# Kernel tuning notes

Measured on AMD Instinct MI355X. Metric: run time of the kernel, lower is better.

The kernel has to match this reference:

```python
import jax, jax.numpy as jnp
import numpy as np

B, RATIO, IN_CH, H = 32, 32, 64, 8
E = IN_CH * H                 # embed_dim = in_channels * n_heads = 512
NODES_PER_GRAPH = 512
N = B * NODES_PER_GRAPH       # 16384 source nodes


def setup_inputs() -> dict:
    key = jax.random.key(0)
    ks = jax.random.split(key, 6)
    x = jax.random.normal(ks[0], (N, E), dtype=jnp.float32)
    # edge_index is accepted by forward but unused in 'attn' mode
    edge_index = jax.random.randint(ks[1], (2, 262144), 0, N, dtype=jnp.int32)
    # per-node graph id, sorted, equal-size graphs (batch[-1] + 1 == B)
    batch = jnp.repeat(jnp.arange(B, dtype=jnp.int32), NODES_PER_GRAPH)
    # learned params: cluster query seeds + MultiheadAttention in/out projections
    xcent_base = jax.random.normal(ks[2], (RATIO, E), dtype=jnp.float32)
    in_proj_w = jax.random.normal(ks[3], (3 * E, E), dtype=jnp.float32) / np.sqrt(E).astype(np.float32)
    in_proj_b = jnp.zeros((3 * E,), dtype=jnp.float32)
    out_proj_w = jax.random.normal(ks[4], (E, E), dtype=jnp.float32) / np.sqrt(E).astype(np.float32)
    out_proj_b = jnp.zeros((E,), dtype=jnp.float32)
    return dict(x=x, edge_index=edge_index, batch=batch, xcent_base=xcent_base,
                in_proj_w=in_proj_w, in_proj_b=in_proj_b,
                out_proj_w=out_proj_w, out_proj_b=out_proj_b)


def reference(x, edge_index, batch, xcent_base, in_proj_w, in_proj_b, out_proj_w, out_proj_b):
    # BipartPool.forward, mode='attn':
    #   x_aggrs = xcent_base.repeat(batch_size, 1)  -> queries [L, E], L = B*ratio
    #   MultiheadAttention(q=x_aggrs, k=v=x, attn_mask=mask[batch].T)
    # mask[batch].T is True (disallowed) where query's graph != node's graph.
    L = B * RATIO
    head_dim = E // H
    x_aggrs = jnp.tile(xcent_base, (B, 1))                        # [L, E]

    wq, wk, wv = jnp.split(in_proj_w, 3, axis=0)                  # each [E, E]
    bq, bk, bv = jnp.split(in_proj_b, 3, axis=0)
    q = (x_aggrs @ wq.T + bq).reshape(L, H, head_dim).transpose(1, 0, 2)  # [H, L, hd]
    k = (x @ wk.T + bk).reshape(N, H, head_dim).transpose(1, 0, 2)        # [H, N, hd]
    v = (x @ wv.T + bv).reshape(N, H, head_dim).transpose(1, 0, 2)        # [H, N, hd]

    batchcent = jnp.repeat(jnp.arange(B, dtype=batch.dtype), RATIO)       # [L]
    allowed = batchcent[:, None] == batch[None, :]                        # [L, N]

    scale = np.float32(1.0 / np.sqrt(head_dim))
    scores = jnp.einsum('hld,hnd->hln', q, k) * scale                     # [H, L, N]
    scores = jnp.where(allowed[None], scores, -jnp.inf)
    attn = jax.nn.softmax(scores, axis=-1)
    out = jnp.einsum('hln,hnd->hld', attn, v)                             # [H, L, hd]
    out = out.transpose(1, 0, 2).reshape(L, E)
    xcent = out @ out_proj_w.T + out_proj_b                               # [L, E]
    # original returns (xcent.reshape(B, ratio, E), None, None, batchcent, None, None)
    return xcent.reshape(B, RATIO, E), batchcent
```

## Files before the change

### kernel.cpp

```cpp
#include <hip/hip_runtime.h>
#include <hip/hip_bf16.h>

#define NGRAPH 32
#define NHEAD 8
#define EMB 512
#define NNODES 16384
#define NPG 512
#define LQ 1024
#define PST 520
#define GCH 262144

typedef __attribute__((ext_vector_type(8))) short short8;
typedef __attribute__((ext_vector_type(4))) float f32x4;

static __device__ __forceinline__ unsigned short f2bf(float f) {
  union { float f; unsigned u; } v; v.f = f;
  unsigned r = (v.u + 0x7fffu + ((v.u >> 16) & 1u)) >> 16;
  return (unsigned short)r;
}

static __device__ __forceinline__ short8 cvt8(float4 a, float4 b) {
  short8 r;
  r[0] = f2bf(a.x); r[1] = f2bf(a.y); r[2] = f2bf(a.z); r[3] = f2bf(a.w);
  r[4] = f2bf(b.x); r[5] = f2bf(b.y); r[6] = f2bf(b.z); r[7] = f2bf(b.w);
  return r;
}

static __device__ __forceinline__ void gload_lds16(const ushort* g, ushort* l) {
  __builtin_amdgcn_global_load_lds(
      (const __attribute__((address_space(1))) unsigned*)g,
      (__attribute__((address_space(3))) unsigned*)l, 16, 0, 0);
}

#define BARRIER_LGKM()                                        \
  do {                                                        \
    asm volatile("s_waitcnt lgkmcnt(0)" ::: "memory");        \
    __builtin_amdgcn_s_barrier();                             \
  } while (0)

__global__ __launch_bounds__(256) void prep_all(
    const float* __restrict__ x, const float* __restrict__ wv,
    const float* __restrict__ wo, const float* __restrict__ wq,
    const float* __restrict__ wk, const float* __restrict__ xc,
    const float* __restrict__ bq,
    ushort* __restrict__ xbC, ushort* __restrict__ xbTC,
    ushort* __restrict__ wvb, ushort* __restrict__ wob,
    ushort* __restrict__ PCb, float* __restrict__ bcent) {
  __shared__ ushort smemU[11776];
  const int b = blockIdx.x;
  const int t = threadIdx.x;

  if (b < 32) {
    ushort* Qs  = smemU;
    ushort* WkT = smemU + 2304;
    int h = b >> 2, qs = b & 3;
    int w = t >> 6, lane = t & 63;
    int lr = lane & 15, grp = lane >> 4, ko = grp * 8;

    {
      int dl = t >> 2, cq = t & 3;
      const float* wr = wk + (long)(h * 64 + dl) * EMB + qs * 128;
#pragma unroll
      for (int m = 0; m < 8; ++m) {
        int c0 = cq * 32 + m * 4;
        float4 v = *reinterpret_cast<const float4*>(wr + c0);
        WkT[(c0 + 0) * 72 + dl] = f2bf(0.125f * v.x);
        WkT[(c0 + 1) * 72 + dl] = f2bf(0.125f * v.y);
        WkT[(c0 + 2) * 72 + dl] = f2bf(0.125f * v.z);
        WkT[(c0 + 3) * 72 + dl] = f2bf(0.125f * v.w);
      }
    }

    f32x4 qa[2];
    qa[0] = (f32x4)(0.0f); qa[1] = (f32x4)(0.0f);
#pragma unroll 4
    for (int kk = 0; kk < EMB; kk += 32) {
      const float* xr0 = xc + lr * EMB + kk + ko;
      const float* xr1 = xc + (16 + lr) * EMB + kk + ko;
      const float* wr  = wq + (long)(h * 64 + w * 16 + lr) * EMB + kk + ko;
      short8 a0 = cvt8(*reinterpret_cast<const float4*>(xr0),
                       *reinterpret_cast<const float4*>(xr0 + 4));
      short8 a1 = cvt8(*reinterpret_cast<const float4*>(xr1),
                       *reinterpret_cast<const float4*>(xr1 + 4));
      short8 bb = cvt8(*reinterpret_cast<const float4*>(wr),
                       *reinterpret_cast<const float4*>(wr + 4));
      qa[0] = __builtin_amdgcn_mfma_f32_16x16x32_bf16(a0, bb, qa[0], 0, 0, 0);
      qa[1] = __builtin_amdgcn_mfma_f32_16x16x32_bf16(a1, bb, qa[1], 0, 0, 0);
    }
    float bias = bq[h * 64 + w * 16 + lr];
#pragma unroll
    for (int i = 0; i < 2; ++i)
#pragma unroll
      for (int r = 0; r < 4; ++r)
        Qs[(i * 16 + grp * 4 + r) * 72 + w * 16 + lr] = f2bf(qa[i][r] + bias);
    __syncthreads();

    f32x4 pa[2][2];
#pragma unroll
    for (int i = 0; i < 2; ++i)
#pragma unroll
      for (int j = 0; j < 2; ++j) pa[i][j] = (f32x4)(0.0f);
#pragma unroll
    for (int kk = 0; kk < 64; kk += 32) {
      short8 a0 = *reinterpret_cast<const short8*>(&Qs[lr * 72 + kk + ko]);
      short8 a1 = *reinterpret_cast<const short8*>(&Qs[(16 + lr) * 72 + kk + ko]);
#pragma unroll
      for (int j = 0; j < 2; ++j) {
        short8 bb = *reinterpret_cast<const short8*>(
            &WkT[(w * 32 + j * 16 + lr) * 72 + kk + ko]);
        pa[0][j] = __builtin_amdgcn_mfma_f32_16x16x32_bf16(a0, bb, pa[0][j], 0, 0, 0);
        pa[1][j] = __builtin_amdgcn_mfma_f32_16x16x32_bf16(a1, bb, pa[1][j], 0, 0, 0);
      }
    }
#pragma unroll
    for (int i = 0; i < 2; ++i)
#pragma unroll
      for (int j = 0; j < 2; ++j)
#pragma unroll
        for (int r = 0; r < 4; ++r)
          PCb[(long)(h * 32 + i * 16 + grp * 4 + r) * EMB + qs * 128 + w * 32 + j * 16 + lr] =
              f2bf(pa[i][j][r]);
    return;
  }

  if (b < 1056) {
    ushort* tileA = smemU;
    ushort* tileB = smemU + 4608;
    int local = b - 32;
    int xr = local & 7, j = local >> 3;
    int m = j >> 5, r = j & 31;
    int g = xr + 8 * m;
    int bc = r & 7;
    int bl = r >> 3;
    int n0 = bl * 128, e0 = bc * 64;
    int trr = t >> 4, tc = t & 15;

    float4 vA[4], vB[4];
#pragma unroll
    for (int p = 0; p < 4; ++p)
      vA[p] = *reinterpret_cast<const float4*>(
          x + (long)(g * NPG + n0 + trr + p * 16) * EMB + e0 + tc * 4);
#pragma unroll
    for (int p = 0; p < 4; ++p)
      vB[p] = *reinterpret_cast<const float4*>(
          x + (long)(g * NPG + n0 + 64 + trr + p * 16) * EMB + e0 + tc * 4);
#pragma unroll
    for (int p = 0; p < 4; ++p) {
      int n = trr + p * 16;
      ushort4 o;
      o.x = f2bf(vA[p].x); o.y = f2bf(vA[p].y); o.z = f2bf(vA[p].z); o.w = f2bf(vA[p].w);
      *reinterpret_cast<ushort4*>(&tileA[n * 72 + tc * 4]) = o;
    }
#pragma unroll
    for (int p = 0; p < 4; ++p) {
      int n = trr + p * 16;
      ushort4 o;
      o.x = f2bf(vB[p].x); o.y = f2bf(vB[p].y); o.z = f2bf(vB[p].z); o.w = f2bf(vB[p].w);
      *reinterpret_cast<ushort4*>(&tileB[n * 72 + tc * 4]) = o;
    }
    __syncthreads();

    {
      int n = t >> 2, pp = t & 3;
#pragma unroll
      for (int tb = 0; tb < 2; ++tb) {
        const ushort* tile = tb ? tileB : tileA;
        int ng = n0 + tb * 64 + n;
        int sp = pp ^ ((ng >> 1) & 3);
#pragma unroll
        for (int kcq = 0; kcq < 2; ++kcq) {
          int kc = bc * 2 + kcq;
          short8 v = *reinterpret_cast<const short8*>(&tile[n * 72 + kcq * 32 + sp * 8]);
          *reinterpret_cast<short8*>(
              &xbC[(long)g * GCH + kc * 16384 + ng * 32 + pp * 8]) = v;
        }
      }
    }
    {
      int e = t >> 2;
      int eg = e0 + e;
      int sp2 = (t & 3) ^ ((eg >> 1) & 3);
      int rot = t & 7;
#pragma unroll
      for (int tb = 0; tb < 2; ++tb) {
        const ushort* tile = tb ? tileB : tileA;
#pragma unroll
        for (int ncq = 0; ncq < 2; ++ncq) {
          int nc = bl * 4 + tb * 2 + ncq;
          ushort tmp[8];
#pragma unroll
          for (int k = 0; k < 8; ++k) {
            int jj = (k + rot) & 7;
            tmp[jj] = tile[(ncq * 32 + sp2 * 8 + jj) * 72 + e];
          }
          *reinterpret_cast<short8*>(
              &xbTC[(long)g * GCH + nc * 16384 + eg * 32 + (t & 3) * 8]) =
              *reinterpret_cast<short8*>(tmp);
        }
      }
    }
    return;
  }

  if (b < 1568) {
    int off = b - 1056;
    const float* src = (off < 256) ? wv : wo;
    ushort* dst = (off < 256) ? wvb : wob;
    off &= 255;
    int i = (off * 256 + t) * 4;
    float4 v = *reinterpret_cast<const float4*>(src + i);
    ushort4 o;
    o.x = f2bf(v.x); o.y = f2bf(v.y); o.z = f2bf(v.z); o.w = f2bf(v.w);
    *reinterpret_cast<ushort4*>(dst + i) = o;
    return;
  }

#pragma unroll
  for (int p = 0; p < 4; ++p) bcent[t + p * 256] = (float)((t + p * 256) >> 5);
}

__global__ __launch_bounds__(1024) void fused_attn(
    const ushort* __restrict__ PCb, const ushort* __restrict__ xbC,
    const ushort* __restrict__ xbTC, const ushort* __restrict__ wvb,
    const float* __restrict__ bvb, ushort* __restrict__ aout) {
  __shared__ ushort PCl[32 * PST];
  __shared__ ushort PBuf[32 * PST];
  __shared__ ushort Bbuf[2][16384];
  __shared__ float rmax[32][16];
  __shared__ float rsum[32][16];

  const int g = blockIdx.x & 31, h = blockIdx.x >> 5;
  const int t = threadIdx.x, w = t >> 6, lane = t & 63;
  const int lr = lane & 15, grp = lane >> 4;
  const int koU = grp * 8;

  const ushort* xgC  = xbC  + (long)g * GCH;
  const ushort* xgTC = xbTC + (long)g * GCH;

  auto STAGE1 = [&](int c, int db) {
#pragma unroll
    for (int q = 0; q < 2; ++q)
      gload_lds16(xgC + c * 16384 + (w * 32 + q * 16) * 32 + lane * 8,
                  &Bbuf[db][(w * 32 + q * 16) * 32]);
  };
  auto STAGE3 = [&](int c, int db) {
#pragma unroll
    for (int q = 0; q < 2; ++q)
      gload_lds16(xgTC + c * 16384 + (w * 32 + q * 16) * 32 + lane * 8,
                  &Bbuf[db][(w * 32 + q * 16) * 32]);
  };

  STAGE1(0, 0);
  STAGE1(1, 1);
  {
    const ushort* pc = PCb + h * 32 * EMB;
#pragma unroll
    for (int p = 0; p < 2; ++p) {
      int u = t + p * 1024;
      int row = u >> 6, col = (u & 63) * 8;
      *reinterpret_cast<short8*>(&PCl[row * PST + col]) =
          *reinterpret_cast<const short8*>(pc + row * EMB + col);
    }
  }
  BARRIER_LGKM();

  f32x4 acc[2][2];
#pragma unroll
  for (int i = 0; i < 2; ++i)
#pragma unroll
    for (int j = 0; j < 2; ++j) acc[i][j] = (f32x4)(0.0f);

#pragma unroll
  for (int c = 0; c < 16; ++c) {
    const int db = c & 1;
    asm volatile("s_waitcnt vmcnt(2)" ::: "memory");
    __builtin_amdgcn_sched_barrier(0);
    short8 a0 = *reinterpret_cast<const short8*>(&PCl[lr * PST + c * 32 + koU]);
    short8 a1 = *reinterpret_cast<const short8*>(&PCl[(16 + lr) * PST + c * 32 + koU]);
    short8 bv8[2];
#pragma unroll
    for (int j = 0; j < 2; ++j) {
      int n = w * 32 + j * 16 + lr;
      int psrc = grp ^ ((n >> 1) & 3);
      bv8[j] = *reinterpret_cast<const short8*>(&Bbuf[db][n * 32 + psrc * 8]);
    }
#pragma unroll
    for (int j = 0; j < 2; ++j) {
      acc[0][j] = __builtin_amdgcn_mfma_f32_16x16x32_bf16(a0, bv8[j], acc[0][j], 0, 0, 0);
      acc[1][j] = __builtin_amdgcn_mfma_f32_16x16x32_bf16(a1, bv8[j], acc[1][j], 0, 0, 0);
    }
    __builtin_amdgcn_sched_barrier(0);
    if (c < 14) STAGE1(c + 2, db);
    else        STAGE3(c - 14, db);
  }

#pragma unroll
  for (int i = 0; i < 2; ++i)
#pragma unroll
    for (int r = 0; r < 4; ++r) {
      float m = fmaxf(acc[i][0][r], acc[i][1][r]);
      m = fmaxf(m, __shfl_xor(m, 1)); m = fmaxf(m, __shfl_xor(m, 2));
      m = fmaxf(m, __shfl_xor(m, 4)); m = fmaxf(m, __shfl_xor(m, 8));
      if (lr == 0) rmax[i * 16 + grp * 4 + r][w] = m;
    }
  BARRIER_LGKM();
#pragma unroll
  for (int i = 0; i < 2; ++i)
#pragma unroll
    for (int r = 0; r < 4; ++r) {
      int row = i * 16 + grp * 4 + r;
      float m = rmax[row][0];
#pragma unroll
      for (int q = 1; q < 16; ++q) m = fmaxf(m, rmax[row][q]);
      float s = 0.f;
#pragma unroll
      for (int j = 0; j < 2; ++j) {
        float e = __expf(acc[i][j][r] - m);
        acc[i][j][r] = e;
        s += e;
      }
      s += __shfl_xor(s, 1); s += __shfl_xor(s, 2);
      s += __shfl_xor(s, 4); s += __shfl_xor(s, 8);
      if (lr == 0) rsum[row][w] = s;
    }
  BARRIER_LGKM();
#pragma unroll
  for (int i = 0; i < 2; ++i)
#pragma unroll
    for (int r = 0; r < 4; ++r) {
      int row = i * 16 + grp * 4 + r;
      float tot = rsum[row][0];
#pragma unroll
      for (int q = 1; q < 16; ++q) tot += rsum[row][q];
      float inv = 1.f / tot;
#pragma unroll
      for (int j = 0; j < 2; ++j)
        PBuf[row * PST + w * 32 + j * 16 + lr] = f2bf(acc[i][j][r] * inv);
    }
  BARRIER_LGKM();

  f32x4 acc2[2][2];
#pragma unroll
  for (int i = 0; i < 2; ++i)
#pragma unroll
    for (int j = 0; j < 2; ++j) acc2[i][j] = (f32x4)(0.0f);

#pragma unroll
  for (int c = 0; c < 16; ++c) {
    const int db = c & 1;
    if (c < 15) asm volatile("s_waitcnt vmcnt(2)" ::: "memory");
    else        asm volatile("s_waitcnt vmcnt(0)" ::: "memory");
    __builtin_amdgcn_sched_barrier(0);
    short8 a0 = *reinterpret_cast<const short8*>(&PBuf[lr * PST + c * 32 + koU]);
    short8 a1 = *reinterpret_cast<const short8*>(&PBuf[(16 + lr) * PST + c * 32 + koU]);
    short8 bv8[2];
#pragma unroll
    for (int j = 0; j < 2; ++j) {
      int e = w * 32 + j * 16 + lr;
      int psrc = grp ^ ((e >> 1) & 3);
      bv8[j] = *reinterpret_cast<const short8*>(&Bbuf[db][e * 32 + psrc * 8]);
    }
#pragma unroll
    for (int j = 0; j < 2; ++j) {
      acc2[0][j] = __builtin_amdgcn_mfma_f32_16x16x32_bf16(a0, bv8[j], acc2[0][j], 0, 0, 0);
      acc2[1][j] = __builtin_amdgcn_mfma_f32_16x16x32_bf16(a1, bv8[j], acc2[1][j], 0, 0, 0);
    }
    __builtin_amdgcn_sched_barrier(0);
    if (c < 14) STAGE3(c + 2, db);
  }
  BARRIER_LGKM();

#pragma unroll
  for (int i = 0; i < 2; ++i)
#pragma unroll
    for (int r = 0; r < 4; ++r) {
      int row = i * 16 + grp * 4 + r;
#pragma unroll
      for (int j = 0; j < 2; ++j)
        PBuf[row * PST + w * 32 + j * 16 + lr] = f2bf(acc2[i][j][r]);
    }
  BARRIER_LGKM();

  if (w < 8) {
    int wr = w >> 2, wc = w & 3;
    f32x4 acc3 = (f32x4)(0.0f);
    const ushort* wvh = wvb + (long)(h * 64 + wc * 16) * EMB;
#pragma unroll
    for (int c = 0; c < 16; ++c) {
      short8 a = *reinterpret_cast<const short8*>(&PBuf[(wr * 16 + lr) * PST + c * 32 + koU]);
      short8 b = *reinterpret_cast<const short8*>(wvh + (long)lr * EMB + c * 32 + koU);
      acc3 = __builtin_amdgcn_mfma_f32_16x16x32_bf16(a, b, acc3, 0, 0, 0);
    }
    float bias = bvb[h * 64 + wc * 16 + lr];
#pragma unroll
    for (int r = 0; r < 4; ++r) {
      int row = wr * 16 + grp * 4 + r;
      aout[(long)(g * 32 + row) * EMB + h * 64 + wc * 16 + lr] = f2bf(acc3[r] + bias);
    }
  }
}

template <int KK, int FM, int FN, int WM, int WN, bool OUT_BF16, bool HAS_BIAS>
__global__ void gemm_abt(const ushort* __restrict__ A, const ushort* __restrict__ Bm,
                         void* __restrict__ C, const float* __restrict__ bias,
                         int lda, int ldb, int ldc) {
  int tid = threadIdx.x;
  int wave = tid >> 6, lane = tid & 63;
  int wr = wave / WN, wc = wave % WN;
  int rowBase = blockIdx.y * (WM * FM * 16) + wr * FM * 16;
  int colBase = blockIdx.x * (WN * FN * 16) + wc * FN * 16;
  int lr = lane & 15;
  int ko = (lane >> 4) * 8;

  f32x4 acc[FM][FN];
#pragma unroll
  for (int i = 0; i < FM; ++i)
#pragma unroll
    for (int j = 0; j < FN; ++j) acc[i][j] = (f32x4)(0.0f);

#pragma unroll 8
  for (int kk = 0; kk < KK; kk += 32) {
    short8 av[FM], bv[FN];
#pragma unroll
    for (int i = 0; i < FM; ++i)
      av[i] = *reinterpret_cast<const short8*>(A + (long)(rowBase + i * 16 + lr) * lda + kk + ko);
#pragma unroll
    for (int j = 0; j < FN; ++j)
      bv[j] = *reinterpret_cast<const short8*>(Bm + (long)(colBase + j * 16 + lr) * ldb + kk + ko);
#pragma unroll
    for (int i = 0; i < FM; ++i)
#pragma unroll
      for (int j = 0; j < FN; ++j)
        acc[i][j] = __builtin_amdgcn_mfma_f32_16x16x32_bf16(av[i], bv[j], acc[i][j], 0, 0, 0);
  }

  int or0 = (lane >> 4) * 4;
#pragma unroll
  for (int i = 0; i < FM; ++i) {
#pragma unroll
    for (int j = 0; j < FN; ++j) {
      int col = colBase + j * 16 + lr;
      float bval = HAS_BIAS ? bias[col] : 0.f;
#pragma unroll
      for (int r = 0; r < 4; ++r) {
        int row = rowBase + i * 16 + or0 + r;
        float v = acc[i][j][r] + bval;
        if (OUT_BF16)
          ((ushort*)C)[(long)row * ldc + col] = f2bf(v);
        else
          ((float*)C)[(long)row * ldc + col] = v;
      }
    }
  }
}

extern "C" void kernel_launch(void* const* d_in, const int* in_sizes, int n_in,
                              void* d_out, int out_size, void* d_ws, size_t ws_size,
                              hipStream_t stream) {
  const float* x          = (const float*)d_in[0];
  const float* xcent_base = (const float*)d_in[3];
  const float* in_proj_w  = (const float*)d_in[4];
  const float* in_proj_b  = (const float*)d_in[5];
  const float* out_proj_w = (const float*)d_in[6];
  const float* out_proj_b = (const float*)d_in[7];

  char* w = (char*)d_ws;
  ushort* xbC  = (ushort*)(w);
  ushort* xbTC = (ushort*)(w + 16777216);
  ushort* PCb  = (ushort*)(w + 33554432);
  ushort* wvb  = (ushort*)(w + 33816576);
  ushort* wob  = (ushort*)(w + 34340864);
  ushort* aout = (ushort*)(w + 34865152);

  const float* wq = in_proj_w;
  const float* wk = in_proj_w + 512 * 512;
  const float* wv = in_proj_w + 1024 * 512;
  const float* bq = in_proj_b;
  const float* bv = in_proj_b + 1024;

  prep_all<<<1569, 256, 0, stream>>>(x, wv, out_proj_w, wq, wk, xcent_base, bq,
                                     xbC, xbTC, wvb, wob, PCb,
                                     (float*)d_out + (long)LQ * EMB);

  fused_attn<<<256, 1024, 0, stream>>>(PCb, xbC, xbTC, wvb, bv, aout);

  gemm_abt<512, 1, 2, 2, 2, false, true><<<dim3(8, 32, 1), 256, 0, stream>>>(
      aout, wob, d_out, out_proj_b, 512, 512, 512);
}
```

Measured before the change: 57.12 us.

## Fuse prep, attention and output projection into one cooperative kernel

Merges the three launches (prep, fused attention, output GEMM) into a single cooperative kernel of 256 blocks of 1024 threads, with grid.sync between phases. Prep work is remapped so each block's four 256-thread sub-groups do the former 256-thread blocks' work. The output projection is redone with a split-K of two wave groups reduced through shared memory. This removes launch gaps and tail effects between kernels, but adds grid-wide barriers and lower prep parallelism per block, and limits the whole grid to 256 co-resident blocks.

```diff
diff --git a/kernel.cpp b/kernel.cpp
--- a/kernel.cpp
+++ b/kernel.cpp
@@ -1,5 +1,8 @@
 #include <hip/hip_runtime.h>
 #include <hip/hip_bf16.h>
+#include <hip/hip_cooperative_groups.h>
+
+namespace cg = cooperative_groups;
 
 #define NGRAPH 32
 #define NHEAD 8
@@ -38,27 +41,121 @@
     __builtin_amdgcn_s_barrier();                             \
   } while (0)
 
-__global__ __launch_bounds__(256) void prep_all(
+struct SmemA {
+  ushort PCl[32 * PST];
+  ushort PBuf[32 * PST];
+  ushort Bbuf[2][16384];
+  float rmax[32][16];
+  float rsum[32][16];
+};
+union SmemU {
+  SmemA a;
+  ushort prep[4][11776];
+};
+
+__global__ __launch_bounds__(1024) void mega(
     const float* __restrict__ x, const float* __restrict__ wv,
     const float* __restrict__ wo, const float* __restrict__ wq,
     const float* __restrict__ wk, const float* __restrict__ xc,
-    const float* __restrict__ bq,
+    const float* __restrict__ bq, const float* __restrict__ bvb,
+    const float* __restrict__ bob,
     ushort* __restrict__ xbC, ushort* __restrict__ xbTC,
     ushort* __restrict__ wvb, ushort* __restrict__ wob,
-    ushort* __restrict__ PCb, float* __restrict__ bcent) {
-  __shared__ ushort smemU[11776];
+    ushort* __restrict__ PCb, ushort* __restrict__ aout,
+    float* __restrict__ outf, float* __restrict__ bcent) {
+  __shared__ __align__(16) SmemU sm;
+  cg::grid_group grid = cg::this_grid();
   const int b = blockIdx.x;
   const int t = threadIdx.x;
-
-  if (b < 32) {
-    ushort* Qs  = smemU;
-    ushort* WkT = smemU + 2304;
-    int h = b >> 2, qs = b & 3;
-    int w = t >> 6, lane = t & 63;
-    int lr = lane & 15, grp = lane >> 4, ko = grp * 8;
+  const int s = t >> 8, t256 = t & 255;
+  ushort* ps = sm.prep[s];
+
+  {
+    const int g = (b & 7) + 8 * (b >> 6);
+    const int r2 = ((b >> 3) & 7) * 4 + s;
+    ushort* tileA = ps;
+    ushort* tileB = ps + 4608;
+    const int bc = r2 & 7;
+    const int bl = r2 >> 3;
+    const int n0 = bl * 128, e0 = bc * 64;
+    const int trr = t256 >> 4, tc = t256 & 15;
+
+    float4 vA[4], vB[4];
+#pragma unroll
+    for (int p = 0; p < 4; ++p)
+      vA[p] = *reinterpret_cast<const float4*>(
+          x + (long)(g * NPG + n0 + trr + p * 16) * EMB + e0 + tc * 4);
+#pragma unroll
+    for (int p = 0; p < 4; ++p)
+      vB[p] = *reinterpret_cast<const float4*>(
+          x + (long)(g * NPG + n0 + 64 + trr + p * 16) * EMB + e0 + tc * 4);
+#pragma unroll
+    for (int p = 0; p < 4; ++p) {
+      int n = trr + p * 16;
+      ushort4 o;
+      o.x = f2bf(vA[p].x); o.y = f2bf(vA[p].y); o.z = f2bf(vA[p].z); o.w = f2bf(vA[p].w);
+      *reinterpret_cast<ushort4*>(&tileA[n * 72 + tc * 4]) = o;
+    }
+#pragma unroll
+    for (int p = 0; p < 4; ++p) {
+      int n = trr + p * 16;
+      ushort4 o;
+      o.x = f2bf(vB[p].x); o.y = f2bf(vB[p].y); o.z = f2bf(vB[p].z); o.w = f2bf(vB[p].w);
+      *reinterpret_cast<ushort4*>(&tileB[n * 72 + tc * 4]) = o;
+    }
+    __syncthreads();
 
     {
-      int dl = t >> 2, cq = t & 3;
+      int n = t256 >> 2, pp = t256 & 3;
+#pragma unroll
+      for (int tb = 0; tb < 2; ++tb) {
+        const ushort* tile = tb ? tileB : tileA;
+        int ng = n0 + tb * 64 + n;
+        int sp = pp ^ ((ng >> 1) & 3);
+#pragma unroll
+        for (int kcq = 0; kcq < 2; ++kcq) {
+          int kc = bc * 2 + kcq;
+          short8 v = *reinterpret_cast<const short8*>(&tile[n * 72 + kcq * 32 + sp * 8]);
+          *reinterpret_cast<short8*>(
+              &xbC[(long)g * GCH + kc * 16384 + ng * 32 + pp * 8]) = v;
+        }
+      }
+    }
+    {
+      int e = t256 >> 2;
+      int eg = e0 + e;
+      int sp2 = (t256 & 3) ^ ((eg >> 1) & 3);
+      int rot = t256 & 7;
+#pragma unroll
+      for (int tb = 0; tb < 2; ++tb) {
+        const ushort* tile = tb ? tileB : tileA;
+#pragma unroll
+        for (int ncq = 0; ncq < 2; ++ncq) {
+          int nc = bl * 4 + tb * 2 + ncq;
+          ushort tmp[8];
+#pragma unroll
+          for (int k = 0; k < 8; ++k) {
+            int jj = (k + rot) & 7;
+            tmp[jj] = tile[(ncq * 32 + sp2 * 8 + jj) * 72 + e];
+          }
+          *reinterpret_cast<short8*>(
+              &xbTC[(long)g * GCH + nc * 16384 + eg * 32 + (t256 & 3) * 8]) =
+              *reinterpret_cast<short8*>(tmp);
+        }
+      }
+    }
+  }
+  __syncthreads();
+
+  if (b < 8) {
+    ushort* Qs  = ps;
+    ushort* WkT = ps + 2304;
+    const int h = b, qs = s;
+    const int w = t256 >> 6, lane = t256 & 63;
+    const int lr = lane & 15, grp = lane >> 4, ko = grp * 8;
+
+    {
+      int dl = t256 >> 2, cq = t256 & 3;
       const float* wr = wk + (long)(h * 64 + dl) * EMB + qs * 128;
 #pragma unroll
       for (int m = 0; m < 8; ++m) {
@@ -70,7 +167,6 @@
         WkT[(c0 + 3) * 72 + dl] = f2bf(0.125f * v.w);
       }
     }
-
     f32x4 qa[2];
     qa[0] = (f32x4)(0.0f); qa[1] = (f32x4)(0.0f);
 #pragma unroll 4
@@ -120,335 +216,236 @@
         for (int r = 0; r < 4; ++r)
           PCb[(long)(h * 32 + i * 16 + grp * 4 + r) * EMB + qs * 128 + w * 32 + j * 16 + lr] =
               f2bf(pa[i][j][r]);
-    return;
-  }
-
-  if (b < 1056) {
-    ushort* tileA = smemU;
-    ushort* tileB = smemU + 4608;
-    int local = b - 32;
-    int xr = local & 7, j = local >> 3;
-    int m = j >> 5, r = j & 31;
-    int g = xr + 8 * m;
-    int bc = r & 7;
-    int bl = r >> 3;
-    int n0 = bl * 128, e0 = bc * 64;
-    int trr = t >> 4, tc = t & 15;
-
-    float4 vA[4], vB[4];
-#pragma unroll
-    for (int p = 0; p < 4; ++p)
-      vA[p] = *reinterpret_cast<const float4*>(
-          x + (long)(g * NPG + n0 + trr + p * 16) * EMB + e0 + tc * 4);
-#pragma unroll
-    for (int p = 0; p < 4; ++p)
-      vB[p] = *reinterpret_cast<const float4*>(
-          x + (long)(g * NPG + n0 + 64 + trr + p * 16) * EMB + e0 + tc * 4);
-#pragma unroll
-    for (int p = 0; p < 4; ++p) {
-      int n = trr + p * 16;
-      ushort4 o;
-      o.x = f2bf(vA[p].x); o.y = f2bf(vA[p].y); o.z = f2bf(vA[p].z); o.w = f2bf(vA[p].w);
-      *reinterpret_cast<ushort4*>(&tileA[n * 72 + tc * 4]) = o;
-    }
-#pragma unroll
-    for (int p = 0; p < 4; ++p) {
-      int n = trr + p * 16;
-      ushort4 o;
-      o.x = f2bf(vB[p].x); o.y = f2bf(vB[p].y); o.z = f2bf(vB[p].z); o.w = f2bf(vB[p].w);
-      *reinterpret_cast<ushort4*>(&tileB[n * 72 + tc * 4]) = o;
-    }
-    __syncthreads();
-
-    {
-      int n = t >> 2, pp = t & 3;
-#pragma unroll
-      for (int tb = 0; tb < 2; ++tb) {
-        const ushort* tile = tb ? tileB : tileA;
-        int ng = n0 + tb * 64 + n;
-        int sp = pp ^ ((ng >> 1) & 3);
-#pragma unroll
-        for (int kcq = 0; kcq < 2; ++kcq) {
-          int kc = bc * 2 + kcq;
-          short8 v = *reinterpret_cast<const short8*>(&tile[n * 72 + kcq * 32 + sp * 8]);
-          *reinterpret_cast<short8*>(
-              &xbC[(long)g * GCH + kc * 16384 + ng * 32 + pp * 8]) = v;
-        }
-      }
-    }
-    {
-      int e = t >> 2;
-      int eg = e0 + e;
-      int sp2 = (t & 3) ^ ((eg >> 1) & 3);
-      int rot = t & 7;
-#pragma unroll
-      for (int tb = 0; tb < 2; ++tb) {
-        const ushort* tile = tb ? tileB : tileA;
-#pragma unroll
-        for (int ncq = 0; ncq < 2; ++ncq) {
-          int nc = bl * 4 + tb * 2 + ncq;
-          ushort tmp[8];
-#pragma unroll
-          for (int k = 0; k < 8; ++k) {
-            int jj = (k + rot) & 7;
-            tmp[jj] = tile[(ncq * 32 + sp2 * 8 + jj) * 72 + e];
-          }
-          *reinterpret_cast<short8*>(
-              &xbTC[(long)g * GCH + nc * 16384 + eg * 32 + (t & 3) * 8]) =
-              *reinterpret_cast<short8*>(tmp);
-        }
-      }
-    }
-    return;
-  }
-
-  if (b < 1568) {
-    int off = b - 1056;
+  } else if (b < 136) {
+    int off = (b - 8) * 4 + s;
     const float* src = (off < 256) ? wv : wo;
     ushort* dst = (off < 256) ? wvb : wob;
     off &= 255;
-    int i = (off * 256 + t) * 4;
+    int i = (off * 256 + t256) * 4;
     float4 v = *reinterpret_cast<const float4*>(src + i);
     ushort4 o;
     o.x = f2bf(v.x); o.y = f2bf(v.y); o.z = f2bf(v.z); o.w = f2bf(v.w);
     *reinterpret_cast<ushort4*>(dst + i) = o;
-    return;
+  } else if (b == 136 && s == 0) {
+#pragma unroll
+    for (int p = 0; p < 4; ++p) bcent[t256 + p * 256] = (float)((t256 + p * 256) >> 5);
   }
 
-#pragma unroll
-  for (int p = 0; p < 4; ++p) bcent[t + p * 256] = (float)((t + p * 256) >> 5);
-}
-
-__global__ __launch_bounds__(1024) void fused_attn(
-    const ushort* __restrict__ PCb, const ushort* __restrict__ xbC,
-    const ushort* __restrict__ xbTC, const ushort* __restrict__ wvb,
-    const float* __restrict__ bvb, ushort* __restrict__ aout) {
-  __shared__ ushort PCl[32 * PST];
-  __shared__ ushort PBuf[32 * PST];
-  __shared__ ushort Bbuf[2][16384];
-  __shared__ float rmax[32][16];
-  __shared__ float rsum[32][16];
-
-  const int g = blockIdx.x & 31, h = blockIdx.x >> 5;
-  const int t = threadIdx.x, w = t >> 6, lane = t & 63;
-  const int lr = lane & 15, grp = lane >> 4;
-  const int koU = grp * 8;
-
-  const ushort* xgC  = xbC  + (long)g * GCH;
-  const ushort* xgTC = xbTC + (long)g * GCH;
-
-  auto STAGE1 = [&](int c, int db) {
-#pragma unroll
-    for (int q = 0; q < 2; ++q)
-      gload_lds16(xgC + c * 16384 + (w * 32 + q * 16) * 32 + lane * 8,
-                  &Bbuf[db][(w * 32 + q * 16) * 32]);
-  };
-  auto STAGE3 = [&](int c, int db) {
-#pragma unroll
-    for (int q = 0; q < 2; ++q)
-      gload_lds16(xgTC + c * 16384 + (w * 32 + q * 16) * 32 + lane * 8,
-                  &Bbuf[db][(w * 32 + q * 16) * 32]);
-  };
-
-  STAGE1(0, 0);
-  STAGE1(1, 1);
+  grid.sync();
+
   {
-    const ushort* pc = PCb + h * 32 * EMB;
-#pragma unroll
-    for (int p = 0; p < 2; ++p) {
-      int u = t + p * 1024;
-      int row = u >> 6, col = (u & 63) * 8;
-      *reinterpret_cast<short8*>(&PCl[row * PST + col]) =
-          *reinterpret_cast<const short8*>(pc + row * EMB + col);
+    const int g = b & 31, h = b >> 5;
+    const int w = t >> 6, lane = t & 63;
+    const int lr = lane & 15, grp = lane >> 4;
+    const int koU = grp * 8;
+
+    const ushort* xgC  = xbC  + (long)g * GCH;
+    const ushort* xgTC = xbTC + (long)g * GCH;
+
+    auto STAGE1 = [&](int c, int db) {
+#pragma unroll
+      for (int q = 0; q < 2; ++q)
+        gload_lds16(xgC + c * 16384 + (w * 32 + q * 16) * 32 + lane * 8,
+                    &sm.a.Bbuf[db][(w * 32 + q * 16) * 32]);
+    };
+    auto STAGE3 = [&](int c, int db) {
+#pragma unroll
+      for (int q = 0; q < 2; ++q)
+        gload_lds16(xgTC + c * 16384 + (w * 32 + q * 16) * 32 + lane * 8,
+                    &sm.a.Bbuf[db][(w * 32 + q * 16) * 32]);
+    };
+
+    STAGE1(0, 0);
+    STAGE1(1, 1);
+    {
+      const ushort* pc = PCb + h * 32 * EMB;
+#pragma unroll
+      for (int p = 0; p < 2; ++p) {
+        int u = t + p * 1024;
+        int row = u >> 6, col = (u & 63) * 8;
+        *reinterpret_cast<short8*>(&sm.a.PCl[row * PST + col]) =
+            *reinterpret_cast<const short8*>(pc + row * EMB + col);
+      }
+    }
+    BARRIER_LGKM();
+
+    f32x4 acc[2][2];
+#pragma unroll
+    for (int i = 0; i < 2; ++i)
+#pragma unroll
+      for (int j = 0; j < 2; ++j) acc[i][j] = (f32x4)(0.0f);
+
+#pragma unroll
+    for (int c = 0; c < 16; ++c) {
+      const int db = c & 1;
+      asm volatile("s_waitcnt vmcnt(2)" ::: "memory");
+      __builtin_amdgcn_sched_barrier(0);
+      short8 a0 = *reinterpret_cast<const short8*>(&sm.a.PCl[lr * PST + c * 32 + koU]);
+      short8 a1 = *reinterpret_cast<const short8*>(&sm.a.PCl[(16 + lr) * PST + c * 32 + koU]);
+      short8 bv8[2];
+#pragma unroll
+      for (int j = 0; j < 2; ++j) {
+        int n = w * 32 + j * 16 + lr;
+        int psrc = grp ^ ((n >> 1) & 3);
+        bv8[j] = *reinterpret_cast<const short8*>(&sm.a.Bbuf[db][n * 32 + psrc * 8]);
+      }
+#pragma unroll
+      for (int j = 0; j < 2; ++j) {
+        acc[0][j] = __builtin_amdgcn_mfma_f32_16x16x32_bf16(a0, bv8[j], acc[0][j], 0, 0, 0);
+        acc[1][j] = __builtin_amdgcn_mfma_f32_16x16x32_bf16(a1, bv8[j], acc[1][j], 0, 0, 0);
+      }
+      __builtin_amdgcn_sched_barrier(0);
+      if (c < 14) STAGE1(c + 2, db);
+      else        STAGE3(c - 14, db);
+    }
+
+#pragma unroll
+    for (int i = 0; i < 2; ++i)
+#pragma unroll
+      for (int r = 0; r < 4; ++r) {
+        float m = fmaxf(acc[i][0][r], acc[i][1][r]);
+        m = fmaxf(m, __shfl_xor(m, 1)); m = fmaxf(m, __shfl_xor(m, 2));
+        m = fmaxf(m, __shfl_xor(m, 4)); m = fmaxf(m, __shfl_xor(m, 8));
+        if (lr == 0) sm.a.rmax[i * 16 + grp * 4 + r][w] = m;
+      }
+    BARRIER_LGKM();
+#pragma unroll
+    for (int i = 0; i < 2; ++i)
+#pragma unroll
+      for (int r = 0; r < 4; ++r) {
+        int row = i * 16 + grp * 4 + r;
+        float m = sm.a.rmax[row][0];
+#pragma unroll
+        for (int q = 1; q < 16; ++q) m = fmaxf(m, sm.a.rmax[row][q]);
+        float ssum = 0.f;
+#pragma unroll
+        for (int j = 0; j < 2; ++j) {
+          float e = __expf(acc[i][j][r] - m);
+          acc[i][j][r] = e;
+          ssum += e;
+        }
+        ssum += __shfl_xor(ssum, 1); ssum += __shfl_xor(ssum, 2);
+        ssum += __shfl_xor(ssum, 4); ssum += __shfl_xor(ssum, 8);
+        if (lr == 0) sm.a.rsum[row][w] = ssum;
+      }
+    BARRIER_LGKM();
+#pragma unroll
+    for (int i = 0; i < 2; ++i)
+#pragma unroll
+      for (int r = 0; r < 4; ++r) {
+        int row = i * 16 + grp * 4 + r;
+        float tot = sm.a.rsum[row][0];
+#pragma unroll
+        for (int q = 1; q < 16; ++q) tot += sm.a.rsum[row][q];
+        float inv = 1.f / tot;
+#pragma unroll
+        for (int j = 0; j < 2; ++j)
+          sm.a.PBuf[row * PST + w * 32 + j * 16 + lr] = f2bf(acc[i][j][r] * inv);
+      }
+    BARRIER_LGKM();
+
+    f32x4 acc2[2][2];
+#pragma unroll
+    for (int i = 0; i < 2; ++i)
+#pragma unroll
+      for (int j = 0; j < 2; ++j) acc2[i][j] = (f32x4)(0.0f);
+
+#pragma unroll
+    for (int c = 0; c < 16; ++c) {
+      const int db = c & 1;
+      if (c < 15) asm volatile("s_waitcnt vmcnt(2)" ::: "memory");
+      else        asm volatile("s_waitcnt vmcnt(0)" ::: "memory");
+      __builtin_amdgcn_sched_barrier(0);
+      short8 a0 = *reinterpret_cast<const short8*>(&sm.a.PBuf[lr * PST + c * 32 + koU]);
+      short8 a1 = *reinterpret_cast<const short8*>(&sm.a.PBuf[(16 + lr) * PST + c * 32 + koU]);
+      short8 bv8[2];
+#pragma unroll
+      for (int j = 0; j < 2; ++j) {
+        int e = w * 32 + j * 16 + lr;
+        int psrc = grp ^ ((e >> 1) & 3);
+        bv8[j] = *reinterpret_cast<const short8*>(&sm.a.Bbuf[db][e * 32 + psrc * 8]);
+      }
+#pragma unroll
+      for (int j = 0; j < 2; ++j) {
+        acc2[0][j] = __builtin_amdgcn_mfma_f32_16x16x32_bf16(a0, bv8[j], acc2[0][j], 0, 0, 0);
+        acc2[1][j] = __builtin_amdgcn_mfma_f32_16x16x32_bf16(a1, bv8[j], acc2[1][j], 0, 0, 0);
+      }
+      __builtin_amdgcn_sched_barrier(0);
+      if (c < 14) STAGE3(c + 2, db);
+    }
+    BARRIER_LGKM();
+
+#pragma unroll
+    for (int i = 0; i < 2; ++i)
+#pragma unroll
+      for (int r = 0; r < 4; ++r) {
+        int row = i * 16 + grp * 4 + r;
+#pragma unroll
+        for (int j = 0; j < 2; ++j)
+          sm.a.PBuf[row * PST + w * 32 + j * 16 + lr] = f2bf(acc2[i][j][r]);
+      }
+    BARRIER_LGKM();
+
+    if (w < 8) {
+      int wr = w >> 2, wc = w & 3;
+      f32x4 acc3 = (f32x4)(0.0f);
+      const ushort* wvh = wvb + (long)(h * 64 + wc * 16) * EMB;
+#pragma unroll
+      for (int c = 0; c < 16; ++c) {
+        short8 a = *reinterpret_cast<const short8*>(&sm.a.PBuf[(wr * 16 + lr) * PST + c * 32 + koU]);
+        short8 bb = *reinterpret_cast<const short8*>(wvh + (long)lr * EMB + c * 32 + koU);
+        acc3 = __builtin_amdgcn_mfma_f32_16x16x32_bf16(a, bb, acc3, 0, 0, 0);
+      }
+      float bias = bvb[h * 64 + wc * 16 + lr];
+#pragma unroll
+      for (int r = 0; r < 4; ++r) {
+        int row = wr * 16 + grp * 4 + r;
+        aout[(long)(g * 32 + row) * EMB + h * 64 + wc * 16 + lr] = f2bf(acc3[r] + bias);
+      }
     }
   }
-  BARRIER_LGKM();
-
-  f32x4 acc[2][2];
-#pragma unroll
-  for (int i = 0; i < 2; ++i)
-#pragma unroll
-    for (int j = 0; j < 2; ++j) acc[i][j] = (f32x4)(0.0f);
-
-#pragma unroll
-  for (int c = 0; c < 16; ++c) {
-    const int db = c & 1;
-    asm volatile("s_waitcnt vmcnt(2)" ::: "memory");
-    __builtin_amdgcn_sched_barrier(0);
-    short8 a0 = *reinterpret_cast<const short8*>(&PCl[lr * PST + c * 32 + koU]);
-    short8 a1 = *reinterpret_cast<const short8*>(&PCl[(16 + lr) * PST + c * 32 + koU]);
-    short8 bv8[2];
-#pragma unroll
-    for (int j = 0; j < 2; ++j) {
-      int n = w * 32 + j * 16 + lr;
-      int psrc = grp ^ ((n >> 1) & 3);
-      bv8[j] = *reinterpret_cast<const short8*>(&Bbuf[db][n * 32 + psrc * 8]);
-    }
-#pragma unroll
-    for (int j = 0; j < 2; ++j) {
-      acc[0][j] = __builtin_amdgcn_mfma_f32_16x16x32_bf16(a0, bv8[j], acc[0][j], 0, 0, 0);
-      acc[1][j] = __builtin_amdgcn_mfma_f32_16x16x32_bf16(a1, bv8[j], acc[1][j], 0, 0, 0);
-    }
-    __builtin_amdgcn_sched_barrier(0);
-    if (c < 14) STAGE1(c + 2, db);
-    else        STAGE3(c - 14, db);
-  }
-
-#pragma unroll
-  for (int i = 0; i < 2; ++i)
-#pragma unroll
-    for (int r = 0; r < 4; ++r) {
-      float m = fmaxf(acc[i][0][r], acc[i][1][r]);
-      m = fmaxf(m, __shfl_xor(m, 1)); m = fmaxf(m, __shfl_xor(m, 2));
-      m = fmaxf(m, __shfl_xor(m, 4)); m = fmaxf(m, __shfl_xor(m, 8));
-      if (lr == 0) rmax[i * 16 + grp * 4 + r][w] = m;
-    }
-  BARRIER_LGKM();
-#pragma unroll
-  for (int i = 0; i < 2; ++i)
-#pragma unroll
-    for (int r = 0; r < 4; ++r) {
-      int row = i * 16 + grp * 4 + r;
-      float m = rmax[row][0];
-#pragma unroll
-      for (int q = 1; q < 16; ++q) m = fmaxf(m, rmax[row][q]);
-      float s = 0.f;
-#pragma unroll
-      for (int j = 0; j < 2; ++j) {
-        float e = __expf(acc[i][j][r] - m);
-        acc[i][j][r] = e;
-        s += e;
-      }
-      s += __shfl_xor(s, 1); s += __shfl_xor(s, 2);
-      s += __shfl_xor(s, 4); s += __shfl_xor(s, 8);
-      if (lr == 0) rsum[row][w] = s;
-    }
-  BARRIER_LGKM();
-#pragma unroll
-  for (int i = 0; i < 2; ++i)
-#pragma unroll
-    for (int r = 0; r < 4; ++r) {
-      int row = i * 16 + grp * 4 + r;
-      float tot = rsum[row][0];
-#pragma unroll
-      for (int q = 1; q < 16; ++q) tot += rsum[row][q];
-      float inv = 1.f / tot;
-#pragma unroll
-      for (int j = 0; j < 2; ++j)
-        PBuf[row * PST + w * 32 + j * 16 + lr] = f2bf(acc[i][j][r] * inv);
-    }
-  BARRIER_LGKM();
-
-  f32x4 acc2[2][2];
-#pragma unroll
-  for (int i = 0; i < 2; ++i)
-#pragma unroll
-    for (int j = 0; j < 2; ++j) acc2[i][j] = (f32x4)(0.0f);
-
-#pragma unroll
-  for (int c = 0; c < 16; ++c) {
-    const int db = c & 1;
-    if (c < 15) asm volatile("s_waitcnt vmcnt(2)" ::: "memory");
-    else        asm volatile("s_waitcnt vmcnt(0)" ::: "memory");
-    __builtin_amdgcn_sched_barrier(0);
-    short8 a0 = *reinterpret_cast<const short8*>(&PBuf[lr * PST + c * 32 + koU]);
-    short8 a1 = *reinterpret_cast<const short8*>(&PBuf[(16 + lr) * PST + c * 32 + koU]);
-    short8 bv8[2];
-#pragma unroll
-    for (int j = 0; j < 2; ++j) {
-      int e = w * 32 + j * 16 + lr;
-      int psrc = grp ^ ((e >> 1) & 3);
-      bv8[j] = *reinterpret_cast<const short8*>(&Bbuf[db][e * 32 + psrc * 8]);
-    }
-#pragma unroll
-    for (int j = 0; j < 2; ++j) {
-      acc2[0][j] = __builtin_amdgcn_mfma_f32_16x16x32_bf16(a0, bv8[j], acc2[0][j], 0, 0, 0);
-      acc2[1][j] = __builtin_amdgcn_mfma_f32_16x16x32_bf16(a1, bv8[j], acc2[1][j], 0, 0, 0);
-    }
-    __builtin_amdgcn_sched_barrier(0);
-    if (c < 14) STAGE3(c + 2, db);
-  }
-  BARRIER_LGKM();
-
-#pragma unroll
-  for (int i = 0; i < 2; ++i)
-#pragma unroll
-    for (int r = 0; r < 4; ++r) {
-      int row = i * 16 + grp * 4 + r;
-#pragma unroll
-      for (int j = 0; j < 2; ++j)
-        PBuf[row * PST + w * 32 + j * 16 + lr] = f2bf(acc2[i][j][r]);
-    }
-  BARRIER_LGKM();
-
-  if (w < 8) {
-    int wr = w >> 2, wc = w & 3;
-    f32x4 acc3 = (f32x4)(0.0f);
-    const ushort* wvh = wvb + (long)(h * 64 + wc * 16) * EMB;
-#pragma unroll
-    for (int c = 0; c < 16; ++c) {
-      short8 a = *reinterpret_cast<const short8*>(&PBuf[(wr * 16 + lr) * PST + c * 32 + koU]);
-      short8 b = *reinterpret_cast<const short8*>(wvh + (long)lr * EMB + c * 32 + koU);
-      acc3 = __builtin_amdgcn_mfma_f32_16x16x32_bf16(a, b, acc3, 0, 0, 0);
-    }
-    float bias = bvb[h * 64 + wc * 16 + lr];
-#pragma unroll
-    for (int r = 0; r < 4; ++r) {
-      int row = wr * 16 + grp * 4 + r;
-      aout[(long)(g * 32 + row) * EMB + h * 64 + wc * 16 + lr] = f2bf(acc3[r] + bias);
-    }
-  }
-}
-
-template <int KK, int FM, int FN, int WM, int WN, bool OUT_BF16, bool HAS_BIAS>
-__global__ void gemm_abt(const ushort* __restrict__ A, const ushort* __restrict__ Bm,
-                         void* __restrict__ C, const float* __restrict__ bias,
-                         int lda, int ldb, int ldc) {
-  int tid = threadIdx.x;
-  int wave = tid >> 6, lane = tid & 63;
-  int wr = wave / WN, wc = wave % WN;
-  int rowBase = blockIdx.y * (WM * FM * 16) + wr * FM * 16;
-  int colBase = blockIdx.x * (WN * FN * 16) + wc * FN * 16;
-  int lr = lane & 15;
-  int ko = (lane >> 4) * 8;
-
-  f32x4 acc[FM][FN];
-#pragma unroll
-  for (int i = 0; i < FM; ++i)
-#pragma unroll
-    for (int j = 0; j < FN; ++j) acc[i][j] = (f32x4)(0.0f);
-
-#pragma unroll 8
-  for (int kk = 0; kk < KK; kk += 32) {
-    short8 av[FM], bv[FN];
-#pragma unroll
-    for (int i = 0; i < FM; ++i)
-      av[i] = *reinterpret_cast<const short8*>(A + (long)(rowBase + i * 16 + lr) * lda + kk + ko);
-#pragma unroll
-    for (int j = 0; j < FN; ++j)
-      bv[j] = *reinterpret_cast<const short8*>(Bm + (long)(colBase + j * 16 + lr) * ldb + kk + ko);
-#pragma unroll
-    for (int i = 0; i < FM; ++i)
-#pragma unroll
-      for (int j = 0; j < FN; ++j)
-        acc[i][j] = __builtin_amdgcn_mfma_f32_16x16x32_bf16(av[i], bv[j], acc[i][j], 0, 0, 0);
-  }
-
-  int or0 = (lane >> 4) * 4;
-#pragma unroll
-  for (int i = 0; i < FM; ++i) {
-#pragma unroll
-    for (int j = 0; j < FN; ++j) {
-      int col = colBase + j * 16 + lr;
-      float bval = HAS_BIAS ? bias[col] : 0.f;
-#pragma unroll
-      for (int r = 0; r < 4; ++r) {
-        int row = rowBase + i * 16 + or0 + r;
-        float v = acc[i][j][r] + bval;
-        if (OUT_BF16)
-          ((ushort*)C)[(long)row * ldc + col] = f2bf(v);
-        else
-          ((float*)C)[(long)row * ldc + col] = v;
+
+  grid.sync();
+
+  {
+    float* gacc = (float*)sm.a.PBuf;
+    const int bx = b & 7, by = b >> 3;
+    const int wave = t >> 6, lane = t & 63;
+    const int lr = lane & 15, ko = (lane >> 4) * 8;
+    const int kg = wave >> 2, w4 = wave & 3;
+    const int wr = w4 >> 1, wc = w4 & 1;
+    const int rowBase = by * 32 + wr * 16;
+    const int colBase = bx * 64 + wc * 32;
+    f32x4 acc0 = (f32x4)(0.0f), acc1 = (f32x4)(0.0f);
+    if (wave < 8) {
+#pragma unroll 4
+      for (int kk = kg * 256; kk < kg * 256 + 256; kk += 32) {
+        short8 av = *reinterpret_cast<const short8*>(aout + (long)(rowBase + lr) * EMB + kk + ko);
+        short8 b0 = *reinterpret_cast<const short8*>(wob + (long)(colBase + lr) * EMB + kk + ko);
+        short8 b1 = *reinterpret_cast<const short8*>(wob + (long)(colBase + 16 + lr) * EMB + kk + ko);
+        acc0 = __builtin_amdgcn_mfma_f32_16x16x32_bf16(av, b0, acc0, 0, 0, 0);
+        acc1 = __builtin_amdgcn_mfma_f32_16x16x32_bf16(av, b1, acc1, 0, 0, 0);
+      }
+      if (kg == 1) {
+        int or0 = (lane >> 4) * 4;
+#pragma unroll
+        for (int r = 0; r < 4; ++r) {
+          gacc[(wr * 16 + or0 + r) * 64 + wc * 32 + lr] = acc0[r];
+          gacc[(wr * 16 + or0 + r) * 64 + wc * 32 + 16 + lr] = acc1[r];
+        }
+      }
+    }
+    __syncthreads();
+    if (wave < 4) {
+      int or0 = (lane >> 4) * 4;
+#pragma unroll
+      for (int r = 0; r < 4; ++r) {
+        int lrow = wr * 16 + or0 + r;
+        int c0 = wc * 32 + lr, c1 = c0 + 16;
+        outf[(long)(by * 32 + lrow) * EMB + bx * 64 + c0] =
+            acc0[r] + gacc[lrow * 64 + c0] + bob[bx * 64 + c0];
+        outf[(long)(by * 32 + lrow) * EMB + bx * 64 + c1] =
+            acc1[r] + gacc[lrow * 64 + c1] + bob[bx * 64 + c1];
       }
     }
   }
@@ -458,11 +455,11 @@
                               void* d_out, int out_size, void* d_ws, size_t ws_size,
                               hipStream_t stream) {
   const float* x          = (const float*)d_in[0];
-  const float* xcent_base = (const float*)d_in[3];
+  const float* xc         = (const float*)d_in[3];
   const float* in_proj_w  = (const float*)d_in[4];
   const float* in_proj_b  = (const float*)d_in[5];
-  const float* out_proj_w = (const float*)d_in[6];
-  const float* out_proj_b = (const float*)d_in[7];
+  const float* wo         = (const float*)d_in[6];
+  const float* bob        = (const float*)d_in[7];
 
   char* w = (char*)d_ws;
   ushort* xbC  = (ushort*)(w);
@@ -472,18 +469,20 @@
   ushort* wob  = (ushort*)(w + 34340864);
   ushort* aout = (ushort*)(w + 34865152);
 
-  const float* wq = in_proj_w;
-  const float* wk = in_proj_w + 512 * 512;
-  const float* wv = in_proj_w + 1024 * 512;
-  const float* bq = in_proj_b;
-  const float* bv = in_proj_b + 1024;
-
-  prep_all<<<1569, 256, 0, stream>>>(x, wv, out_proj_w, wq, wk, xcent_base, bq,
-                                     xbC, xbTC, wvb, wob, PCb,
-                                     (float*)d_out + (long)LQ * EMB);
-
-  fused_attn<<<256, 1024, 0, stream>>>(PCb, xbC, xbTC, wvb, bv, aout);
-
-  gemm_abt<512, 1, 2, 2, 2, false, true><<<dim3(8, 32, 1), 256, 0, stream>>>(
-      aout, wob, d_out, out_proj_b, 512, 512, 512);
+  const float* wq  = in_proj_w;
+  const float* wk  = in_proj_w + 512 * 512;
+  const float* wv  = in_proj_w + 1024 * 512;
+  const float* bq  = in_proj_b;
+  const float* bvb = in_proj_b + 1024;
+  float* outf  = (float*)d_out;
+  float* bcent = (float*)d_out + (long)LQ * EMB;
+
+  void* args[] = {
+      (void*)&x,   (void*)&wv,  (void*)&wo,   (void*)&wq,  (void*)&wk,
+      (void*)&xc,  (void*)&bq,  (void*)&bvb,  (void*)&bob,
+      (void*)&xbC, (void*)&xbTC,(void*)&wvb,  (void*)&wob, (void*)&PCb,
+      (void*)&aout,(void*)&outf,(void*)&bcent};
+
+  hipLaunchCooperativeKernel((const void*)mega, dim3(256), dim3(1024),
+                             args, 0, stream);
 }
```

New measurement: 167.6 us. +193.5%, slower.
